# Performance work log

Hardware: AMD Instinct MI355X
Metric: run time of the kernel (lower is better)

Reference implementation:

```python
import jax, jax.numpy as jnp
import numpy as np

B = 32768
D_IN = 512
D_OUT = 512
N_DIGITS = 9
N_LEVELS = N_DIGITS + 1


def _xavier_uniform(key, shape, gain):
    # nn.init.xavier_uniform_ on Linear weight of shape (out, in)
    fan_out, fan_in = shape
    limit = gain * np.sqrt(6.0 / (fan_in + fan_out))
    return jax.random.uniform(key, shape, jnp.float32, -limit, limit)


def setup_inputs() -> dict:
    key = jax.random.key(0)
    kx, kv, *kw = jax.random.split(key, 2 + N_LEVELS)
    x = jax.random.normal(kx, (B, D_IN), dtype=jnp.float32)
    valuations = jax.random.randint(kv, (B,), 0, N_LEVELS, dtype=jnp.int64)
    # level-aware xavier init: gain = 1/(1 + 0.1*level)
    W = jnp.stack([
        _xavier_uniform(kw[l], (D_OUT, D_IN), 1.0 / (1.0 + 0.1 * l))
        for l in range(N_LEVELS)
    ], axis=0)  # (L, out, in)
    level_gates = jnp.ones((N_LEVELS,), dtype=jnp.float32)
    cross_level_attn = (jnp.eye(N_LEVELS, dtype=jnp.float32) * 0.9
                        + jnp.ones((N_LEVELS, N_LEVELS), dtype=jnp.float32) * 0.01)
    bias = jnp.zeros((D_OUT,), dtype=jnp.float32)
    return {"x": x, "valuations": valuations, "W": W,
            "level_gates": level_gates, "cross_level_attn": cross_level_attn,
            "bias": bias}


def reference(x, valuations, W, level_gates, cross_level_attn, bias):
    val = jnp.clip(valuations, 0, N_DIGITS)  # (B,)
    # 10 per-level linears as one batched GEMM: (B, L, out)
    level_outputs = jnp.einsum('bi,loi->blo', x, W)
    gates = jax.nn.sigmoid(level_gates)  # (L,)
    level_outputs = level_outputs * gates[None, :, None]
    # per-sample gather of own valuation level -> (B, out)
    output = jnp.take_along_axis(level_outputs, val[:, None, None], axis=1)[:, 0, :]
    # soft cross-level attention combine
    attn_weights = jax.nn.softmax(cross_level_attn[val], axis=-1)  # (B, L)
    weighted = jnp.einsum('bl,blo->bo', attn_weights, level_outputs)
    output = 0.7 * output + 0.3 * weighted
    return output + bias
```

## Files before the change

### kernel.cpp

```cpp
#include <hip/hip_runtime.h>

#define B_N 32768
#define D 512
#define DD (D * D)
#define NLEV 10
#define TM 128
#define TN 256
#define BK 32
#define NITER (D / BK)
#define NHB 128
#define MROWS_MAX 34048
#define MAX_RT (MROWS_MAX / TM)

typedef unsigned short u16;
typedef short s16x8 __attribute__((ext_vector_type(8)));
typedef u16 u16x8 __attribute__((ext_vector_type(8)));
typedef float f32x4 __attribute__((ext_vector_type(4)));

__device__ __forceinline__ u16 f2bf(float f) {
  union { float f; unsigned u; } v; v.f = f;
  unsigned r = v.u + 0x7fffu + ((v.u >> 16) & 1u);
  return (u16)(r >> 16);
}
__device__ __forceinline__ int clampv(int v) {
  return v < 0 ? 0 : (v > NLEV - 1 ? NLEV - 1 : v);
}

__global__ void k1(const float* __restrict__ W, const float* __restrict__ lg,
                   const float* __restrict__ attn, const int* __restrict__ val,
                   u16* __restrict__ weff, u16* __restrict__ hist,
                   int* __restrict__ perm) {
  const int t = threadIdx.x;
  if (blockIdx.x < DD / 256) {
    __shared__ float c[NLEV * NLEV];
    if (t < NLEV) {
      float g[NLEV], a[NLEV], mx = -1e30f;
      #pragma unroll
      for (int l = 0; l < NLEV; ++l) {
        g[l] = 1.0f / (1.0f + expf(-lg[l]));
        a[l] = attn[t * NLEV + l];
        mx = fmaxf(mx, a[l]);
      }
      float s = 0.f;
      #pragma unroll
      for (int l = 0; l < NLEV; ++l) { a[l] = expf(a[l] - mx); s += a[l]; }
      float inv = 1.0f / s;
      #pragma unroll
      for (int l = 0; l < NLEV; ++l) {
        float cc = 0.3f * a[l] * inv * g[l];
        if (l == t) cc += 0.7f * g[t];
        c[t * NLEV + l] = cc;
      }
    }
    __syncthreads();
    const int idx = blockIdx.x * 256 + t;
    float w[NLEV];
    #pragma unroll
    for (int l = 0; l < NLEV; ++l) w[l] = W[l * DD + idx];
    #pragma unroll
    for (int v = 0; v < NLEV; ++v) {
      float s = 0.f;
      #pragma unroll
      for (int l = 0; l < NLEV; ++l) s += c[v * NLEV + l] * w[l];
      weff[v * DD + idx] = f2bf(s);
    }
  } else {
    __shared__ int lc[NLEV];
    const int b = blockIdx.x - DD / 256;
    if (t < NLEV) lc[t] = 0;
    __syncthreads();
    const int gid = b * 256 + t;
    atomicAdd(&lc[clampv(val[gid])], 1);
    perm[gid] = -1;
    if (b < (MROWS_MAX - B_N) / 256) perm[B_N + b * 256 + t] = -1;
    __syncthreads();
    if (t < NLEV) hist[b * NLEV + t] = (u16)lc[t];
  }
}

__global__ void k2(const int* __restrict__ val, const u16* __restrict__ hist,
                   int* __restrict__ perm, int* __restrict__ starts) {
  __shared__ int h[NHB * NLEV];
  __shared__ int st[NLEV + 1];
  __shared__ int cnt[NLEV];
  __shared__ int lc[NLEV];
  const int t = threadIdx.x, b = blockIdx.x;
  for (int i = t; i < NHB * NLEV; i += 256) h[i] = hist[i];
  if (t < NLEV) lc[t] = 0;
  __syncthreads();
  if (t < NLEV) {
    int run = 0;
    for (int bb = 0; bb < NHB; ++bb) {
      int x = h[bb * NLEV + t];
      h[bb * NLEV + t] = run;
      run += x;
    }
    cnt[t] = run;
  }
  __syncthreads();
  if (t == 0) {
    int s = 0;
    for (int v = 0; v < NLEV; ++v) {
      st[v] = s;
      s += (cnt[v] + TM - 1) & ~(TM - 1);
    }
    st[NLEV] = s;
  }
  __syncthreads();
  const int gid = b * 256 + t;
  const int v = clampv(val[gid]);
  const int pos = atomicAdd(&lc[v], 1);
  perm[st[v] + h[b * NLEV + v] + pos] = gid;
  if (b == 0 && t <= NLEV) starts[t] = st[t];
}

__global__ __launch_bounds__(512, 4) void k3(
    const float* __restrict__ x, const u16* __restrict__ weff,
    const int* __restrict__ perm, const int* __restrict__ starts,
    const float* __restrict__ bias, float* __restrict__ out) {
  __shared__ u16 As[3][TM * BK];
  __shared__ u16 Bs[3][TN * BK];

  const int ct = blockIdx.x, rt = blockIdx.y;
  const int Mpad = starts[NLEV];
  if (rt * TM >= Mpad) return;

  int v = 0;
  #pragma unroll
  for (int i = 1; i < NLEV; ++i) if (rt * TM >= starts[i]) v = i;

  const int tid = threadIdx.x;
  const int lane = tid & 63, wave = tid >> 6;
  const int wm = (wave >> 2) * 64, wn = (wave & 3) * 64;
  const int fm = lane & 15;
  const int cb = lane >> 4;

  const int ar = tid >> 2;
  const int ah = tid & 3;
  int prow = perm[rt * TM + ar];
  if (prow < 0) prow = 0;
  const float* xrow = x + (size_t)prow * D + ah * 8;
  const int sw = (ar >> 1) & 3;
  const int aslot = ar * BK + ((ah ^ sw) << 3);

  const u16* wb = weff + ((size_t)v * D + ct * TN) * D;
  const int c0i = wave * 64 + lane;
  const int c1i = 512 + c0i;
  const int n0 = c0i >> 2, s0 = c0i & 3, kc0 = s0 ^ ((n0 >> 1) & 3);
  const int n1 = c1i >> 2, s1 = c1i & 3, kc1 = s1 ^ ((n1 >> 1) & 3);
  const u16* gb0 = wb + n0 * D + kc0 * 8;
  const u16* gb1 = wb + n1 * D + kc1 * 8;
  const int bdst0 = c0i * 8, bdst1 = c1i * 8;

  f32x4 acc[4][4];
  #pragma unroll
  for (int i = 0; i < 4; ++i)
    #pragma unroll
    for (int j = 0; j < 4; ++j) acc[i][j] = (f32x4){0.f, 0.f, 0.f, 0.f};

  {
    const f32x4* xp = (const f32x4*)xrow;
    f32x4 f0 = xp[0], f1 = xp[1];
    u16x8 cc;
    #pragma unroll
    for (int q = 0; q < 4; ++q) { cc[q] = f2bf(f0[q]); cc[4 + q] = f2bf(f1[q]); }
    *(u16x8*)(As[0] + aslot) = cc;
  }
  f32x4 cf0, cf1;
  {
    const f32x4* xp = (const f32x4*)(xrow + BK);
    cf0 = xp[0]; cf1 = xp[1];
  }
  __builtin_amdgcn_global_load_lds(
      (const __attribute__((address_space(1))) void*)gb0,
      (__attribute__((address_space(3))) void*)(Bs[0] + bdst0), 16, 0, 0);
  __builtin_amdgcn_global_load_lds(
      (const __attribute__((address_space(1))) void*)gb1,
      (__attribute__((address_space(3))) void*)(Bs[0] + bdst1), 16, 0, 0);
  __builtin_amdgcn_global_load_lds(
      (const __attribute__((address_space(1))) void*)(gb0 + BK),
      (__attribute__((address_space(3))) void*)(Bs[1] + bdst0), 16, 0, 0);
  __builtin_amdgcn_global_load_lds(
      (const __attribute__((address_space(1))) void*)(gb1 + BK),
      (__attribute__((address_space(3))) void*)(Bs[1] + bdst1), 16, 0, 0);
  asm volatile("s_waitcnt vmcnt(0)" ::: "memory");
  asm volatile("s_waitcnt lgkmcnt(0)" ::: "memory");
  __builtin_amdgcn_s_barrier();
  __builtin_amdgcn_sched_barrier(0);

  u16 *Ar = (u16*)As[0], *Aw = (u16*)As[1], *Ax = (u16*)As[2];
  u16 *Br = (u16*)Bs[0], *Bm = (u16*)Bs[1], *Bw = (u16*)Bs[2];

  for (int i = 0; i < NITER; ++i) {
    const bool h2 = (i + 2 < NITER);
    const bool hn = (i + 1 < NITER);
    f32x4 nf0, nf1;
    if (h2) {
      const f32x4* xp = (const f32x4*)(xrow + (i + 2) * BK);
      nf0 = xp[0]; nf1 = xp[1];
    }
    if (h2) {
      const int ko = (i + 2) * BK;
      __builtin_amdgcn_global_load_lds(
          (const __attribute__((address_space(1))) void*)(gb0 + ko),
          (__attribute__((address_space(3))) void*)(Bw + bdst0), 16, 0, 0);
      __builtin_amdgcn_global_load_lds(
          (const __attribute__((address_space(1))) void*)(gb1 + ko),
          (__attribute__((address_space(3))) void*)(Bw + bdst1), 16, 0, 0);
    }
    s16x8 af[4], bf[4];
    #pragma unroll
    for (int t4 = 0; t4 < 4; ++t4) {
      const int m = wm + t4 * 16 + fm;
      af[t4] = *(const s16x8*)(Ar + m * BK + ((cb ^ ((m >> 1) & 3)) << 3));
      const int n = wn + t4 * 16 + fm;
      bf[t4] = *(const s16x8*)(Br + n * BK + ((cb ^ ((n >> 1) & 3)) << 3));
    }
    __builtin_amdgcn_s_setprio(1);
    #pragma unroll
    for (int tm = 0; tm < 4; ++tm)
      #pragma unroll
      for (int tn = 0; tn < 4; ++tn)
        acc[tm][tn] = __builtin_amdgcn_mfma_f32_16x16x32_bf16(af[tm], bf[tn], acc[tm][tn], 0, 0, 0);
    __builtin_amdgcn_s_setprio(0);
    if (hn) {
      u16x8 cc;
      #pragma unroll
      for (int q = 0; q < 4; ++q) { cc[q] = f2bf(cf0[q]); cc[4 + q] = f2bf(cf1[q]); }
      *(u16x8*)(Aw + aslot) = cc;
      if (h2) { cf0 = nf0; cf1 = nf1; }
      if (h2) asm volatile("s_waitcnt vmcnt(4)" ::: "memory");
      else    asm volatile("s_waitcnt vmcnt(0)" ::: "memory");
      asm volatile("s_waitcnt lgkmcnt(0)" ::: "memory");
      __builtin_amdgcn_s_barrier();
      __builtin_amdgcn_sched_barrier(0);
      u16* t;
      t = Ar; Ar = Aw; Aw = Ax; Ax = t;
      t = Br; Br = Bm; Bm = Bw; Bw = t;
    }
  }

  float bv[4];
  #pragma unroll
  for (int tn = 0; tn < 4; ++tn) bv[tn] = bias[ct * TN + wn + tn * 16 + fm];
  #pragma unroll
  for (int tm = 0; tm < 4; ++tm) {
    #pragma unroll
    for (int r = 0; r < 4; ++r) {
      const int mrow = wm + tm * 16 + (lane >> 4) * 4 + r;
      const int p2 = perm[rt * TM + mrow];
      if (p2 >= 0) {
        float* o = out + (size_t)p2 * D + ct * TN + wn + fm;
        #pragma unroll
        for (int tn = 0; tn < 4; ++tn)
          o[tn * 16] = acc[tm][tn][r] + bv[tn];
      }
    }
  }
}

extern "C" void kernel_launch(void* const* d_in, const int* in_sizes, int n_in,
                              void* d_out, int out_size, void* d_ws, size_t ws_size,
                              hipStream_t stream) {
  const float* x    = (const float*)d_in[0];
  const int*   val  = (const int*)d_in[1];
  const float* W    = (const float*)d_in[2];
  const float* lg   = (const float*)d_in[3];
  const float* attn = (const float*)d_in[4];
  const float* bias = (const float*)d_in[5];
  float* out = (float*)d_out;

  char* ws = (char*)d_ws;
  int* starts = (int*)(ws + 0);
  u16* hist   = (u16*)(ws + 64);
  int* perm   = (int*)(ws + 2688);
  u16* weff   = (u16*)(ws + 139264);

  k1<<<DD / 256 + NHB, 256, 0, stream>>>(W, lg, attn, val, weff, hist, perm);
  k2<<<NHB, 256, 0, stream>>>(val, hist, perm, starts);
  k3<<<dim3(D / TN, MAX_RT), 512, 0, stream>>>(x, weff, perm, starts, bias, out);
}
```

Baseline: 171.8 us.

## Pre-convert x to bf16 in k1 and stream A tiles via global_load_lds

Adds extra blocks to the first kernel that convert all of x to a bf16 workspace buffer. The GEMM kernel then loads A tiles straight into LDS with asynchronous global-to-LDS loads, mirroring the B path. This removes the per-iteration fp32 register loads, bf16 conversion and LDS stores from the main loop, and halves the A bytes read per tile. In exchange it adds a separate pass that reads x and writes a bf16 copy (about 32 MB of fp32 in, 16 MB out), and x is still converted twice for the two column tiles' worth of reads only once now.

```diff
diff --git a/kernel.cpp b/kernel.cpp
--- a/kernel.cpp
+++ b/kernel.cpp
@@ -9,6 +9,7 @@
 #define BK 32
 #define NITER (D / BK)
 #define NHB 128
+#define CONVB 2048
 #define MROWS_MAX 34048
 #define MAX_RT (MROWS_MAX / TM)
 
@@ -28,8 +29,9 @@
 
 __global__ void k1(const float* __restrict__ W, const float* __restrict__ lg,
                    const float* __restrict__ attn, const int* __restrict__ val,
+                   const float* __restrict__ x,
                    u16* __restrict__ weff, u16* __restrict__ hist,
-                   int* __restrict__ perm) {
+                   int* __restrict__ perm, u16* __restrict__ xa) {
   const int t = threadIdx.x;
   if (blockIdx.x < DD / 256) {
     __shared__ float c[NLEV * NLEV];
@@ -64,7 +66,7 @@
       for (int l = 0; l < NLEV; ++l) s += c[v * NLEV + l] * w[l];
       weff[v * DD + idx] = f2bf(s);
     }
-  } else {
+  } else if (blockIdx.x < DD / 256 + NHB) {
     __shared__ int lc[NLEV];
     const int b = blockIdx.x - DD / 256;
     if (t < NLEV) lc[t] = 0;
@@ -75,6 +77,19 @@
     if (b < (MROWS_MAX - B_N) / 256) perm[B_N + b * 256 + t] = -1;
     __syncthreads();
     if (t < NLEV) hist[b * NLEV + t] = (u16)lc[t];
+  } else {
+    const int b2 = blockIdx.x - (DD / 256 + NHB);
+    const size_t base = (size_t)b2 * 8192 + t * 32;
+    const f32x4* xs = (const f32x4*)(x + base);
+    u16x8* xd = (u16x8*)(xa + base);
+    #pragma unroll
+    for (int q = 0; q < 4; ++q) {
+      f32x4 a = xs[2 * q], bqq = xs[2 * q + 1];
+      u16x8 cc;
+      #pragma unroll
+      for (int r = 0; r < 4; ++r) { cc[r] = f2bf(a[r]); cc[4 + r] = f2bf(bqq[r]); }
+      xd[q] = cc;
+    }
   }
 }
 
@@ -115,7 +130,7 @@
 }
 
 __global__ __launch_bounds__(512, 4) void k3(
-    const float* __restrict__ x, const u16* __restrict__ weff,
+    const u16* __restrict__ xa, const u16* __restrict__ weff,
     const int* __restrict__ perm, const int* __restrict__ starts,
     const float* __restrict__ bias, float* __restrict__ out) {
   __shared__ u16 As[3][TM * BK];
@@ -136,12 +151,11 @@
   const int cb = lane >> 4;
 
   const int ar = tid >> 2;
-  const int ah = tid & 3;
+  const int aslt = tid & 3;
   int prow = perm[rt * TM + ar];
   if (prow < 0) prow = 0;
-  const float* xrow = x + (size_t)prow * D + ah * 8;
-  const int sw = (ar >> 1) & 3;
-  const int aslot = ar * BK + ((ah ^ sw) << 3);
+  const u16* ga = xa + (size_t)prow * D + ((aslt ^ ((ar >> 1) & 3)) << 3);
+  const int adst = tid * 8;
 
   const u16* wb = weff + ((size_t)v * D + ct * TN) * D;
   const int c0i = wave * 64 + lane;
@@ -158,25 +172,18 @@
     #pragma unroll
     for (int j = 0; j < 4; ++j) acc[i][j] = (f32x4){0.f, 0.f, 0.f, 0.f};
 
-  {
-    const f32x4* xp = (const f32x4*)xrow;
-    f32x4 f0 = xp[0], f1 = xp[1];
-    u16x8 cc;
-    #pragma unroll
-    for (int q = 0; q < 4; ++q) { cc[q] = f2bf(f0[q]); cc[4 + q] = f2bf(f1[q]); }
-    *(u16x8*)(As[0] + aslot) = cc;
-  }
-  f32x4 cf0, cf1;
-  {
-    const f32x4* xp = (const f32x4*)(xrow + BK);
-    cf0 = xp[0]; cf1 = xp[1];
-  }
+  __builtin_amdgcn_global_load_lds(
+      (const __attribute__((address_space(1))) void*)ga,
+      (__attribute__((address_space(3))) void*)(As[0] + adst), 16, 0, 0);
   __builtin_amdgcn_global_load_lds(
       (const __attribute__((address_space(1))) void*)gb0,
       (__attribute__((address_space(3))) void*)(Bs[0] + bdst0), 16, 0, 0);
   __builtin_amdgcn_global_load_lds(
       (const __attribute__((address_space(1))) void*)gb1,
       (__attribute__((address_space(3))) void*)(Bs[0] + bdst1), 16, 0, 0);
+  __builtin_amdgcn_global_load_lds(
+      (const __attribute__((address_space(1))) void*)(ga + BK),
+      (__attribute__((address_space(3))) void*)(As[1] + adst), 16, 0, 0);
   __builtin_amdgcn_global_load_lds(
       (const __attribute__((address_space(1))) void*)(gb0 + BK),
       (__attribute__((address_space(3))) void*)(Bs[1] + bdst0), 16, 0, 0);
@@ -184,23 +191,19 @@
       (const __attribute__((address_space(1))) void*)(gb1 + BK),
       (__attribute__((address_space(3))) void*)(Bs[1] + bdst1), 16, 0, 0);
   asm volatile("s_waitcnt vmcnt(0)" ::: "memory");
-  asm volatile("s_waitcnt lgkmcnt(0)" ::: "memory");
   __builtin_amdgcn_s_barrier();
   __builtin_amdgcn_sched_barrier(0);
 
-  u16 *Ar = (u16*)As[0], *Aw = (u16*)As[1], *Ax = (u16*)As[2];
-  u16 *Br = (u16*)Bs[0], *Bm = (u16*)Bs[1], *Bw = (u16*)Bs[2];
+  u16 *Arr = (u16*)As[0], *Am = (u16*)As[1], *Aw = (u16*)As[2];
+  u16 *Brr = (u16*)Bs[0], *Bm = (u16*)Bs[1], *Bw = (u16*)Bs[2];
 
   for (int i = 0; i < NITER; ++i) {
     const bool h2 = (i + 2 < NITER);
-    const bool hn = (i + 1 < NITER);
-    f32x4 nf0, nf1;
-    if (h2) {
-      const f32x4* xp = (const f32x4*)(xrow + (i + 2) * BK);
-      nf0 = xp[0]; nf1 = xp[1];
-    }
     if (h2) {
       const int ko = (i + 2) * BK;
+      __builtin_amdgcn_global_load_lds(
+          (const __attribute__((address_space(1))) void*)(ga + ko),
+          (__attribute__((address_space(3))) void*)(Aw + adst), 16, 0, 0);
       __builtin_amdgcn_global_load_lds(
           (const __attribute__((address_space(1))) void*)(gb0 + ko),
           (__attribute__((address_space(3))) void*)(Bw + bdst0), 16, 0, 0);
@@ -212,9 +215,9 @@
     #pragma unroll
     for (int t4 = 0; t4 < 4; ++t4) {
       const int m = wm + t4 * 16 + fm;
-      af[t4] = *(const s16x8*)(Ar + m * BK + ((cb ^ ((m >> 1) & 3)) << 3));
+      af[t4] = *(const s16x8*)(Arr + m * BK + ((cb ^ ((m >> 1) & 3)) << 3));
       const int n = wn + t4 * 16 + fm;
-      bf[t4] = *(const s16x8*)(Br + n * BK + ((cb ^ ((n >> 1) & 3)) << 3));
+      bf[t4] = *(const s16x8*)(Brr + n * BK + ((cb ^ ((n >> 1) & 3)) << 3));
     }
     __builtin_amdgcn_s_setprio(1);
     #pragma unroll
@@ -223,20 +226,15 @@
       for (int tn = 0; tn < 4; ++tn)
         acc[tm][tn] = __builtin_amdgcn_mfma_f32_16x16x32_bf16(af[tm], bf[tn], acc[tm][tn], 0, 0, 0);
     __builtin_amdgcn_s_setprio(0);
-    if (hn) {
-      u16x8 cc;
-      #pragma unroll
-      for (int q = 0; q < 4; ++q) { cc[q] = f2bf(cf0[q]); cc[4 + q] = f2bf(cf1[q]); }
-      *(u16x8*)(Aw + aslot) = cc;
-      if (h2) { cf0 = nf0; cf1 = nf1; }
-      if (h2) asm volatile("s_waitcnt vmcnt(4)" ::: "memory");
+    if (i + 1 < NITER) {
+      if (h2) asm volatile("s_waitcnt vmcnt(3)" ::: "memory");
       else    asm volatile("s_waitcnt vmcnt(0)" ::: "memory");
       asm volatile("s_waitcnt lgkmcnt(0)" ::: "memory");
       __builtin_amdgcn_s_barrier();
       __builtin_amdgcn_sched_barrier(0);
       u16* t;
-      t = Ar; Ar = Aw; Aw = Ax; Ax = t;
-      t = Br; Br = Bm; Bm = Bw; Bw = t;
+      t = Arr; Arr = Am; Am = Aw; Aw = t;
+      t = Brr; Brr = Bm; Bm = Bw; Bw = t;
     }
   }
 
@@ -275,8 +273,10 @@
   u16* hist   = (u16*)(ws + 64);
   int* perm   = (int*)(ws + 2688);
   u16* weff   = (u16*)(ws + 139264);
-
-  k1<<<DD / 256 + NHB, 256, 0, stream>>>(W, lg, attn, val, weff, hist, perm);
+  u16* xa     = (u16*)(ws + 5382144);
+
+  k1<<<DD / 256 + NHB + CONVB, 256, 0, stream>>>(W, lg, attn, val, x,
+                                                 weff, hist, perm, xa);
   k2<<<NHB, 256, 0, stream>>>(val, hist, perm, starts);
-  k3<<<dim3(D / TN, MAX_RT), 512, 0, stream>>>(x, weff, perm, starts, bias, out);
-}
+  k3<<<dim3(D / TN, MAX_RT), 512, 0, stream>>>(xa, weff, perm, starts, bias, out);
+}
```

Result: no change. 174.9 us (+1.8%).
